# Kernel tuning notes

Measured on AMD Instinct MI355X. Metric: run time of the kernel, lower is better.

## Reference

```python
import jax, jax.numpy as jnp
import numpy as np

N_NODES = 50000
N_EDGES = 600000
IN_CH = 128
HID = 256
OUT_FEAT = 256
OUT_CH = 128
EPS = 1e-12


def _sage_conv(x, src, dst, mask_f, Wl, bl, Wr, n_nodes):
    # PyG SAGEConv: out = lin_l(mean_{j in N(i)} x_j) + lin_r(x_i); L2-normalize rows.
    msg = x[src] * mask_f[:, None]                                  # [E, d] gather
    agg = jax.ops.segment_sum(msg, dst, num_segments=n_nodes)      # [N, d]
    cnt = jax.ops.segment_sum(mask_f, dst, num_segments=n_nodes)   # [N]
    agg = agg / jnp.maximum(cnt, 1.0)[:, None]                      # mean over kept edges
    out = agg @ Wl.T + bl + x @ Wr.T                                 # [N, h]
    nrm = jnp.maximum(jnp.linalg.norm(out, axis=-1, keepdims=True), EPS)
    return out / nrm


def setup_inputs() -> dict:
    key = jax.random.key(0)
    ks = jax.random.split(key, 12)
    x = jax.random.normal(ks[0], (N_NODES, IN_CH), dtype=jnp.float32)
    edge_index = jax.random.randint(ks[1], (2, N_EDGES), 0, N_NODES, dtype=jnp.int32)
    edge_mask = jax.random.bernoulli(ks[2], 0.7, (N_EDGES,))  # dropout_edge p=0.3 keep mask

    def lin(k, fan_out, fan_in):
        s = 1.0 / np.sqrt(fan_in)
        return jax.random.uniform(k, (fan_out, fan_in), jnp.float32, -s, s)

    W1l = lin(ks[3], HID, IN_CH)
    b1 = jnp.zeros((HID,), jnp.float32)
    W1r = lin(ks[4], HID, IN_CH)
    Ws = lin(ks[5], HID, IN_CH)
    bs = jnp.zeros((HID,), jnp.float32)
    W2l = lin(ks[6], OUT_FEAT, HID)
    b2 = jnp.zeros((OUT_FEAT,), jnp.float32)
    W2r = lin(ks[7], OUT_FEAT, HID)
    Wo = lin(ks[8], OUT_CH, OUT_FEAT)
    bo = jnp.zeros((OUT_CH,), jnp.float32)
    return {"x": x, "edge_index": edge_index, "edge_mask": edge_mask,
            "W1l": W1l, "b1": b1, "W1r": W1r, "Ws": Ws, "bs": bs,
            "W2l": W2l, "b2": b2, "W2r": W2r, "Wo": Wo, "bo": bo}


def reference(x, edge_index, edge_mask, W1l, b1, W1r, Ws, bs, W2l, b2, W2r, Wo, bo):
    src, dst = edge_index[0], edge_index[1]
    ones = jnp.ones((src.shape[0],), x.dtype)
    # conv1 uses all edges
    h = _sage_conv(x, src, dst, ones, W1l, b1, W1r, N_NODES)
    h = h + (x @ Ws.T + bs)
    h = jnp.tanh(h)
    # conv2 uses edge-dropped graph (mask = kept edges)
    mask_f = edge_mask.astype(x.dtype)
    h = jnp.tanh(_sage_conv(h, src, dst, mask_f, W2l, b2, W2r, N_NODES))
    return h @ Wo.T + bo
```

## Files before the change

kernel.cpp:

```cpp
#include <hip/hip_runtime.h>
#include <hip/hip_bf16.h>

#define N_NODES 50000
#define N_PAD   50048
#define N_EDGES 600000
#define IN_CH 128
#define HID 256
#define OUT_CH 128

typedef unsigned short u16;
typedef unsigned char u8;
typedef unsigned int u32;

typedef __attribute__((ext_vector_type(8))) short short8;
typedef __attribute__((ext_vector_type(4))) float f32x4;

typedef __attribute__((address_space(3))) u32 as3_u32;
typedef __attribute__((address_space(1))) const u32 as1_u32;

__device__ __forceinline__ float bf2f(u16 v) {
    unsigned u = ((unsigned)v) << 16;
    return __uint_as_float(u);
}
__device__ __forceinline__ u16 f2bf(float f) {
    unsigned u = __float_as_uint(f);
    u += 0x7FFF + ((u >> 16) & 1);
    return (u16)(u >> 16);
}

__device__ __forceinline__ void async16(const void* g, void* l) {
    __builtin_amdgcn_global_load_lds((as1_u32*)g, (as3_u32*)l, 16, 0, 0);
}

__global__ void detect_kernel(const u16* __restrict__ xu, const u8* __restrict__ mb,
                              int* __restrict__ flags) {
    int lane = threadIdx.x & 63;

    int inr = 0;
    {
        u32 w0 = ((const u32*)xu)[lane * 2 + 0];
        u32 w1 = ((const u32*)xu)[lane * 2 + 1];
        u16 h[4] = {(u16)w0, (u16)(w0 >> 16), (u16)w1, (u16)(w1 >> 16)};
#pragma unroll
        for (int j = 0; j < 4; j++) {
            int e = (h[j] >> 7) & 0xFF;
            if (e >= 100 && e <= 133) inr++;
        }
    }

    int c1 = 0, c23 = 0, h3f_1 = 0, h3f_3 = 0;
#pragma unroll
    for (int t = 0; t < 16; t++) {
        u32 w = ((const u32*)mb)[t * 64 + lane];
        u8 b1 = (u8)(w >> 8), b2 = (u8)(w >> 16), b3 = (u8)(w >> 24);
        if (b1) c1++;
        if (b1 == 0x3F) h3f_1 = 1;
        if (b2) c23++;
        if (b3) c23++;
        if (b3 == 0x3F) h3f_3 = 1;
    }

#pragma unroll
    for (int off = 32; off > 0; off >>= 1) {
        inr   += __shfl_xor(inr, off, 64);
        c1    += __shfl_xor(c1, off, 64);
        c23   += __shfl_xor(c23, off, 64);
        h3f_1 |= __shfl_xor(h3f_1, off, 64);
        h3f_3 |= __shfl_xor(h3f_3, off, 64);
    }

    if (lane == 0 && blockIdx.x == 0) {
        flags[0] = (inr >= 200) ? 1 : 0;
        int fmt;
        if (h3f_1) fmt = 3;
        else if (h3f_3) fmt = 2;
        else if (c1 + c23 > 0) fmt = 0;
        else fmt = 1;
        flags[1] = fmt;
    }
}

__global__ void biases_kernel(const void* __restrict__ b1, const void* __restrict__ bs,
                              const void* __restrict__ b2, const void* __restrict__ bo,
                              float* __restrict__ dst, const int* __restrict__ flags) {
    int i = blockIdx.x * blockDim.x + threadIdx.x;
    if (i >= 896) return;
    const void* src; int idx;
    if (i < 256)      { src = b1; idx = i; }
    else if (i < 512) { src = bs; idx = i - 256; }
    else if (i < 768) { src = b2; idx = i - 512; }
    else              { src = bo; idx = i - 768; }
    float v;
    if (flags[0]) v = bf2f(((const u16*)src)[idx]);
    else          v = ((const float*)src)[idx];
    dst[i] = v;
}

__global__ void wcat_kernel(const void* __restrict__ A, const void* __restrict__ B,
                            u16* __restrict__ dst, int N, int K1, int K2,
                            const int* __restrict__ flags) {
    int i = blockIdx.x * blockDim.x + threadIdx.x;
    int K = K1 + K2;
    if (i >= N * K) return;
    int n = i / K, k = i % K;
    const void* src; int idx;
    if (k < K1) { src = A; idx = n * K1 + k; }
    else        { src = B; idx = n * K2 + (k - K1); }
    u16 v;
    if (flags[0]) v = ((const u16*)src)[idx];
    else          v = f2bf(((const float*)src)[idx]);
    dst[i] = v;
}

__global__ void hist_kernel(const int* __restrict__ ei, int* __restrict__ deg,
                            int* __restrict__ rank) {
    int i = blockIdx.x * blockDim.x + threadIdx.x;
    if (i >= N_EDGES) return;
    int d = ei[N_EDGES + i];
    rank[i] = atomicAdd(&deg[d], 1);
}

__global__ void partial_kernel(const int* __restrict__ deg, int* __restrict__ partial) {
    __shared__ int sh[256];
    int t = threadIdx.x;
    int i = blockIdx.x * 256 + t;
    sh[t] = (i < N_NODES) ? deg[i] : 0;
    __syncthreads();
    for (int s = 128; s > 0; s >>= 1) {
        if (t < s) sh[t] += sh[t + s];
        __syncthreads();
    }
    if (t == 0) partial[blockIdx.x] = sh[0];
}

__global__ void scanp_kernel(const int* __restrict__ partial, int* __restrict__ pscan, int nb) {
    __shared__ int sh[256];
    int t = threadIdx.x;
    int v = (t < nb) ? partial[t] : 0;
    sh[t] = v;
    __syncthreads();
    for (int o = 1; o < 256; o <<= 1) {
        int u = (t >= o) ? sh[t - o] : 0;
        __syncthreads();
        sh[t] += u;
        __syncthreads();
    }
    if (t < nb) pscan[t] = sh[t] - v;
}

__global__ void rowptr_kernel(const int* __restrict__ deg, const int* __restrict__ pscan,
                              int* __restrict__ row_ptr) {
    __shared__ int sh[256];
    int t = threadIdx.x;
    int i = blockIdx.x * 256 + t;
    int v = (i < N_NODES) ? deg[i] : 0;
    sh[t] = v;
    __syncthreads();
    for (int o = 1; o < 256; o <<= 1) {
        int u = (t >= o) ? sh[t - o] : 0;
        __syncthreads();
        sh[t] += u;
        __syncthreads();
    }
    if (i <= N_NODES) row_ptr[i] = pscan[blockIdx.x] + sh[t] - v;
}

__global__ void scatter_csr_kernel(const int* __restrict__ ei, const int* __restrict__ rank,
                                   const int* __restrict__ row_ptr,
                                   const void* __restrict__ em,
                                   u32* __restrict__ srcs, const int* __restrict__ flags) {
    int i = blockIdx.x * blockDim.x + threadIdx.x;
    if (i >= N_EDGES) return;
    int d = ei[N_EDGES + i];
    int p = row_ptr[d] + rank[i];
    int fmt = flags[1];
    bool keep;
    if (fmt == 0)      keep = ((const u8*)em)[i] != 0;
    else if (fmt == 1) keep = ((const int*)em)[i] != 0;
    else if (fmt == 2) keep = ((const float*)em)[i] != 0.f;
    else               keep = ((const u16*)em)[i] != 0;
    srcs[p] = (u32)ei[i] | (keep ? 0u : 0x80000000u);
}

__global__ __launch_bounds__(256) void gather1_kernel(const int* __restrict__ row_ptr,
                                                      const u32* __restrict__ srcs,
                                                      const u16* __restrict__ xb,
                                                      u16* __restrict__ aggb) {
    int wid = (blockIdx.x * blockDim.x + threadIdx.x) >> 6;
    int lane = threadIdx.x & 63;
    if (wid >= N_NODES) return;
    int start = row_ptr[wid], end = row_ptr[wid + 1];
    float ax = 0.f, ay = 0.f, bx = 0.f, by = 0.f;
    int e = start;
    for (; e + 2 <= end; e += 2) {
        int s0 = (int)(srcs[e] & 0x7fffffffu);
        int s1 = (int)(srcs[e + 1] & 0x7fffffffu);
        u32 v0 = *(const u32*)(xb + (size_t)s0 * IN_CH + lane * 2);
        u32 v1 = *(const u32*)(xb + (size_t)s1 * IN_CH + lane * 2);
        ax += bf2f((u16)v0); ay += bf2f((u16)(v0 >> 16));
        bx += bf2f((u16)v1); by += bf2f((u16)(v1 >> 16));
    }
    if (e < end) {
        int s0 = (int)(srcs[e] & 0x7fffffffu);
        u32 v0 = *(const u32*)(xb + (size_t)s0 * IN_CH + lane * 2);
        ax += bf2f((u16)v0); ay += bf2f((u16)(v0 >> 16));
    }
    float inv = 1.f / fmaxf((float)(end - start), 1.f);
    u32 o = (u32)f2bf((ax + bx) * inv) | ((u32)f2bf((ay + by) * inv) << 16);
    *(u32*)(aggb + (size_t)wid * IN_CH + lane * 2) = o;
}

__global__ __launch_bounds__(256) void gather2_kernel(const int* __restrict__ row_ptr,
                                                      const u32* __restrict__ srcs,
                                                      const u16* __restrict__ h1b,
                                                      u16* __restrict__ aggb) {
    int wid = (blockIdx.x * blockDim.x + threadIdx.x) >> 6;
    int lane = threadIdx.x & 63;
    if (wid >= N_NODES) return;
    int start = row_ptr[wid], end = row_ptr[wid + 1];
    float a0 = 0.f, a1 = 0.f, a2 = 0.f, a3 = 0.f, c = 0.f;
    for (int e = start; e < end; e++) {
        u32 sv = srcs[e];
        if ((int)sv >= 0) {
            const u16* p = h1b + (size_t)sv * HID + lane * 4;
            u32 v0 = *(const u32*)p;
            u32 v1 = *(const u32*)(p + 2);
            a0 += bf2f((u16)v0);
            a1 += bf2f((u16)(v0 >> 16));
            a2 += bf2f((u16)v1);
            a3 += bf2f((u16)(v1 >> 16));
            c += 1.f;
        }
    }
    float inv = 1.f / fmaxf(c, 1.f);
    u32 o0 = (u32)f2bf(a0 * inv) | ((u32)f2bf(a1 * inv) << 16);
    u32 o1 = (u32)f2bf(a2 * inv) | ((u32)f2bf(a3 * inv) << 16);
    u16* p = aggb + (size_t)wid * HID + lane * 4;
    *(u32*)p = o0;
    *(u32*)(p + 2) = o1;
}

template<int MODE>
__global__ __launch_bounds__(256, 2) void gemm_staged(
    const u16* __restrict__ A0, const u16* __restrict__ A1,
    const u16* __restrict__ W0, const u16* __restrict__ W1,
    const float* __restrict__ bias0, const float* __restrict__ bias1,
    u16* __restrict__ outb, void* __restrict__ outv, const int* __restrict__ flags) {

    constexpr int NT  = (MODE == 3) ? 2 : 4;
    constexpr int Nw  = NT * 16;
    constexpr int NKS = (MODE == 1) ? 6 : ((MODE == 2) ? 8 : 4);
    constexpr int BBYTES = NT * 64 * 128;
    __shared__ __align__(16) u8 ldsmem[16384 + 2 * BBYTES];

    int tid = threadIdx.x;
    int w = tid >> 6, lane = tid & 63;
    int q = lane >> 4, c = lane & 15;
    int m_base = blockIdx.x * 64;
    int rj = lane >> 3, jj = lane & 7;
    int j16 = ((jj ^ rj) << 4);

    f32x4 acc[4][NT], acc2[4][NT];
    const f32x4 z = {0.f, 0.f, 0.f, 0.f};
#pragma unroll
    for (int mt = 0; mt < 4; mt++)
#pragma unroll
        for (int nt = 0; nt < NT; nt++) { acc[mt][nt] = z; acc2[mt][nt] = z; }

    auto stage = [&](int ks, int b) {
        const u16* ap; int astr, kta;
        const u16* wp; int wstr, ktw;
        if (MODE == 1) {
            astr = 128;
            if (ks < 2)      { ap = A0; kta = ks; }
            else if (ks < 4) { ap = A1; kta = ks - 2; }
            else             { ap = A1; kta = ks - 4; }
            if (ks < 4) { wp = W0; wstr = 256; ktw = ks; }
            else        { wp = W1; wstr = 128; ktw = ks - 4; }
        } else if (MODE == 2) {
            astr = 256;
            if (ks < 4) { ap = A0; kta = ks; } else { ap = A1; kta = ks - 4; }
            wp = W0; wstr = 512; ktw = ks;
        } else {
            astr = 256; ap = A0; kta = ks;
            wp = W0; wstr = 256; ktw = ks;
        }
#pragma unroll
        for (int t = 0; t < 2; t++) {
            int r = w * 16 + t * 8;
            const u8* g = (const u8*)(ap + (size_t)(m_base + r + rj) * astr) + kta * 128 + j16;
            async16(g, ldsmem + b * 8192 + r * 128);
        }
#pragma unroll
        for (int t = 0; t < NT * 2; t++) {
            int n = w * Nw + t * 8;
            const u8* g = (const u8*)(wp + (size_t)(n + rj) * wstr) + ktw * 128 + j16;
            async16(g, ldsmem + 16384 + b * BBYTES + n * 128);
        }
    };

    auto compute = [&](int b, f32x4 (*tgt)[NT]) {
        const u8* ab = ldsmem + b * 8192;
        const u8* bb = ldsmem + 16384 + b * BBYTES;
#pragma unroll
        for (int kk = 0; kk < 2; kk++) {
            int sA = (((kk * 4 + q) ^ (c & 7)) << 4);
            short8 af[4], bfr[NT];
#pragma unroll
            for (int mt = 0; mt < 4; mt++)
                af[mt] = *(const short8*)(ab + (mt * 16 + c) * 128 + sA);
#pragma unroll
            for (int nt = 0; nt < NT; nt++)
                bfr[nt] = *(const short8*)(bb + (w * Nw + nt * 16 + c) * 128 + sA);
#pragma unroll
            for (int mt = 0; mt < 4; mt++)
#pragma unroll
                for (int nt = 0; nt < NT; nt++)
                    tgt[mt][nt] = __builtin_amdgcn_mfma_f32_16x16x32_bf16(af[mt], bfr[nt], tgt[mt][nt], 0, 0, 0);
        }
    };

    stage(0, 0);
    int b = 0;
#pragma unroll
    for (int ks = 0; ks < NKS; ks++) {
        __syncthreads();
        if (ks + 1 < NKS) stage(ks + 1, b ^ 1);
        if (MODE == 1 && ks >= 4) compute(b, acc2);
        else                      compute(b, acc);
        b ^= 1;
    }
    __syncthreads();

    if (MODE == 3) {
        float bcol[NT];
#pragma unroll
        for (int nt = 0; nt < NT; nt++) bcol[nt] = bias0[w * Nw + nt * 16 + c];
        int isbf = flags[0];
#pragma unroll
        for (int mt = 0; mt < 4; mt++)
#pragma unroll
            for (int r = 0; r < 4; r++) {
                int row = m_base + mt * 16 + q * 4 + r;
                if (row < N_NODES) {
#pragma unroll
                    for (int nt = 0; nt < NT; nt++) {
                        float v = acc[mt][nt][r] + bcol[nt];
                        int col = w * Nw + nt * 16 + c;
                        if (isbf) ((u16*)outv)[(size_t)row * OUT_CH + col] = f2bf(v);
                        else      ((float*)outv)[(size_t)row * OUT_CH + col] = v;
                    }
                }
            }
    } else {
        float* redf = (float*)ldsmem;
        float bcol[NT], b2col[NT];
#pragma unroll
        for (int nt = 0; nt < NT; nt++) {
            int col = w * Nw + nt * 16 + c;
            bcol[nt] = bias0[col];
            if (MODE == 1) b2col[nt] = bias1[col];
        }
        float s[4][4];
#pragma unroll
        for (int mt = 0; mt < 4; mt++)
#pragma unroll
            for (int r = 0; r < 4; r++) {
                float t = 0.f;
#pragma unroll
                for (int nt = 0; nt < NT; nt++) {
                    float v = acc[mt][nt][r] + bcol[nt];
                    acc[mt][nt][r] = v;
                    t += v * v;
                }
                s[mt][r] = t;
            }
#pragma unroll
        for (int off = 1; off < 16; off <<= 1) {
#pragma unroll
            for (int mt = 0; mt < 4; mt++)
#pragma unroll
                for (int r = 0; r < 4; r++)
                    s[mt][r] += __shfl_xor(s[mt][r], off, 64);
        }
        if (c == 0) {
#pragma unroll
            for (int mt = 0; mt < 4; mt++)
#pragma unroll
                for (int r = 0; r < 4; r++)
                    redf[(mt * 16 + q * 4 + r) * 4 + w] = s[mt][r];
        }
        __syncthreads();
        if (tid < 64) {
            float t = redf[tid * 4] + redf[tid * 4 + 1] + redf[tid * 4 + 2] + redf[tid * 4 + 3];
            redf[256 + tid] = 1.f / fmaxf(sqrtf(t), 1e-12f);
        }
        __syncthreads();
#pragma unroll
        for (int mt = 0; mt < 4; mt++)
#pragma unroll
            for (int r = 0; r < 4; r++) {
                int rl = mt * 16 + q * 4 + r;
                int row = m_base + rl;
                if (row < N_NODES) {
                    float iv = redf[256 + rl];
#pragma unroll
                    for (int nt = 0; nt < NT; nt++) {
                        int col = w * Nw + nt * 16 + c;
                        float h;
                        if (MODE == 1) h = acc[mt][nt][r] * iv + acc2[mt][nt][r] + b2col[nt];
                        else           h = acc[mt][nt][r] * iv;
                        outb[(size_t)row * HID + col] = f2bf(tanhf(h));
                    }
                }
            }
    }
}

extern "C" void kernel_launch(void* const* d_in, const int* in_sizes, int n_in,
                              void* d_out, int out_size, void* d_ws, size_t ws_size,
                              hipStream_t stream) {
    const void* x    = d_in[0];
    const int*  ei   = (const int*)d_in[1];
    const void* em   = d_in[2];
    const void* W1l  = d_in[3];
    const void* b1   = d_in[4];
    const void* W1r  = d_in[5];
    const void* Ws   = d_in[6];
    const void* bs   = d_in[7];
    const void* W2l  = d_in[8];
    const void* b2   = d_in[9];
    const void* W2r  = d_in[10];
    const void* Wo   = d_in[11];
    const void* bo   = d_in[12];

    char* p = (char*)d_ws;
    auto carve = [&](size_t bytes) { char* r = p; p += (bytes + 63) & ~(size_t)63; return r; };
    int*   flags  = (int*)carve(256);
    u16*   xb     = (u16*)carve((size_t)N_PAD * IN_CH * 2);
    u16*   h1b    = (u16*)carve((size_t)N_PAD * HID * 2);
    u16*   aggb   = (u16*)carve((size_t)N_PAD * HID * 2);
    u16*   h2b    = (u16*)carve((size_t)N_PAD * HID * 2);
    u16*   Wc1    = (u16*)carve(256 * 256 * 2);
    u16*   Wsb    = (u16*)carve(256 * 128 * 2);
    u16*   Wc2    = (u16*)carve(256 * 512 * 2);
    u16*   Wob    = (u16*)carve(128 * 256 * 2);
    float* biasf  = (float*)carve(896 * 4);
    int*   deg    = (int*)carve(50056 * 4);
    int*   row_ptr= (int*)carve(50056 * 4);
    int*   partial= (int*)carve(256 * 4);
    int*   pscan  = (int*)carve(256 * 4);
    int*   rank   = (int*)carve((size_t)N_EDGES * 4);
    u32*   srcs   = (u32*)carve((size_t)N_EDGES * 4);
    float* b1f = biasf, *bsf = biasf + 256, *b2f = biasf + 512, *bof = biasf + 768;
    (void)ws_size; (void)in_sizes; (void)n_in; (void)out_size;

    detect_kernel<<<1, 64, 0, stream>>>((const u16*)x, (const u8*)em, flags);

    wcat_kernel<<<(N_NODES * IN_CH + 255) / 256, 256, 0, stream>>>(x, x, xb, 1, N_NODES * IN_CH, 0, flags);
    wcat_kernel<<<(256 * 256 + 255) / 256, 256, 0, stream>>>(W1l, W1r, Wc1, 256, 128, 128, flags);
    wcat_kernel<<<(256 * 128 + 255) / 256, 256, 0, stream>>>(Ws, Ws, Wsb, 1, 256 * 128, 0, flags);
    wcat_kernel<<<(256 * 512 + 255) / 256, 256, 0, stream>>>(W2l, W2r, Wc2, 256, 256, 256, flags);
    wcat_kernel<<<(128 * 256 + 255) / 256, 256, 0, stream>>>(Wo, Wo, Wob, 1, 128 * 256, 0, flags);
    biases_kernel<<<4, 256, 0, stream>>>(b1, bs, b2, bo, biasf, flags);

    hipMemsetAsync(deg, 0, 50056 * sizeof(int), stream);
    hist_kernel<<<(N_EDGES + 255) / 256, 256, 0, stream>>>(ei, deg, rank);
    const int NB = (N_NODES + 255) / 256;
    partial_kernel<<<NB, 256, 0, stream>>>(deg, partial);
    scanp_kernel<<<1, 256, 0, stream>>>(partial, pscan, NB);
    rowptr_kernel<<<NB, 256, 0, stream>>>(deg, pscan, row_ptr);
    scatter_csr_kernel<<<(N_EDGES + 255) / 256, 256, 0, stream>>>(ei, rank, row_ptr, em, srcs, flags);

    const int GB = N_PAD / 64;

    gather1_kernel<<<(N_NODES * 64) / 256, 256, 0, stream>>>(row_ptr, srcs, xb, aggb);
    gemm_staged<1><<<GB, 256, 0, stream>>>(aggb, xb, Wc1, Wsb, b1f, bsf, h1b, nullptr, flags);

    gather2_kernel<<<(N_NODES * 64) / 256, 256, 0, stream>>>(row_ptr, srcs, h1b, aggb);
    gemm_staged<2><<<GB, 256, 0, stream>>>(aggb, h1b, Wc2, nullptr, b2f, nullptr, h2b, nullptr, flags);

    gemm_staged<3><<<GB, 256, 0, stream>>>(h2b, nullptr, Wob, nullptr, bof, nullptr, nullptr, d_out, flags);
}
```

Measured before the change: 352.0 us.

## Build separate masked CSR and preload neighbor indices per wave with readlane

Builds a second CSR containing only kept edges, so the second gather no longer branches on a mask bit per edge and drops masked edges entirely. Both gather kernels load up to 64 neighbor indices in one coalesced per-lane read and broadcast them with readlane instead of issuing scalar loads per edge. The second gather also unrolls by two with uint2 loads to get more memory requests in flight. In exchange the CSR build does a second atomic histogram, doubles the scan work and writes an extra index array.

```diff
diff --git a/kernel.cpp b/kernel.cpp
--- a/kernel.cpp
+++ b/kernel.cpp
@@ -112,129 +112,166 @@
     dst[i] = v;
 }
 
-__global__ void hist_kernel(const int* __restrict__ ei, int* __restrict__ deg,
-                            int* __restrict__ rank) {
+__global__ void hist_kernel(const int* __restrict__ ei, const void* __restrict__ em,
+                            int* __restrict__ deg, int* __restrict__ deg2,
+                            int* __restrict__ rank, int* __restrict__ krank,
+                            const int* __restrict__ flags) {
     int i = blockIdx.x * blockDim.x + threadIdx.x;
     if (i >= N_EDGES) return;
     int d = ei[N_EDGES + i];
     rank[i] = atomicAdd(&deg[d], 1);
-}
-
-__global__ void partial_kernel(const int* __restrict__ deg, int* __restrict__ partial) {
-    __shared__ int sh[256];
-    int t = threadIdx.x;
-    int i = blockIdx.x * 256 + t;
-    sh[t] = (i < N_NODES) ? deg[i] : 0;
-    __syncthreads();
-    for (int s = 128; s > 0; s >>= 1) {
-        if (t < s) sh[t] += sh[t + s];
-        __syncthreads();
-    }
-    if (t == 0) partial[blockIdx.x] = sh[0];
-}
-
-__global__ void scanp_kernel(const int* __restrict__ partial, int* __restrict__ pscan, int nb) {
-    __shared__ int sh[256];
-    int t = threadIdx.x;
-    int v = (t < nb) ? partial[t] : 0;
-    sh[t] = v;
-    __syncthreads();
-    for (int o = 1; o < 256; o <<= 1) {
-        int u = (t >= o) ? sh[t - o] : 0;
-        __syncthreads();
-        sh[t] += u;
-        __syncthreads();
-    }
-    if (t < nb) pscan[t] = sh[t] - v;
-}
-
-__global__ void rowptr_kernel(const int* __restrict__ deg, const int* __restrict__ pscan,
-                              int* __restrict__ row_ptr) {
-    __shared__ int sh[256];
-    int t = threadIdx.x;
-    int i = blockIdx.x * 256 + t;
-    int v = (i < N_NODES) ? deg[i] : 0;
-    sh[t] = v;
-    __syncthreads();
-    for (int o = 1; o < 256; o <<= 1) {
-        int u = (t >= o) ? sh[t - o] : 0;
-        __syncthreads();
-        sh[t] += u;
-        __syncthreads();
-    }
-    if (i <= N_NODES) row_ptr[i] = pscan[blockIdx.x] + sh[t] - v;
-}
-
-__global__ void scatter_csr_kernel(const int* __restrict__ ei, const int* __restrict__ rank,
-                                   const int* __restrict__ row_ptr,
-                                   const void* __restrict__ em,
-                                   u32* __restrict__ srcs, const int* __restrict__ flags) {
-    int i = blockIdx.x * blockDim.x + threadIdx.x;
-    if (i >= N_EDGES) return;
-    int d = ei[N_EDGES + i];
-    int p = row_ptr[d] + rank[i];
     int fmt = flags[1];
     bool keep;
     if (fmt == 0)      keep = ((const u8*)em)[i] != 0;
     else if (fmt == 1) keep = ((const int*)em)[i] != 0;
     else if (fmt == 2) keep = ((const float*)em)[i] != 0.f;
     else               keep = ((const u16*)em)[i] != 0;
-    srcs[p] = (u32)ei[i] | (keep ? 0u : 0x80000000u);
+    krank[i] = keep ? atomicAdd(&deg2[d], 1) : -1;
+}
+
+__global__ void partial_kernel(const int* __restrict__ deg, const int* __restrict__ deg2,
+                               int* __restrict__ partial, int nb) {
+    __shared__ int sh[256];
+    int t = threadIdx.x;
+    int arr = (blockIdx.x >= nb) ? 1 : 0;
+    int blk = blockIdx.x - arr * nb;
+    const int* d = arr ? deg2 : deg;
+    int i = blk * 256 + t;
+    sh[t] = (i < N_NODES) ? d[i] : 0;
+    __syncthreads();
+    for (int s = 128; s > 0; s >>= 1) {
+        if (t < s) sh[t] += sh[t + s];
+        __syncthreads();
+    }
+    if (t == 0) partial[blockIdx.x] = sh[0];
+}
+
+__global__ void scanp_kernel(const int* __restrict__ partial, int* __restrict__ pscan, int nb) {
+    __shared__ int sh[256];
+    int t = threadIdx.x;
+    int base = blockIdx.x * nb;
+    int v = (t < nb) ? partial[base + t] : 0;
+    sh[t] = v;
+    __syncthreads();
+    for (int o = 1; o < 256; o <<= 1) {
+        int u = (t >= o) ? sh[t - o] : 0;
+        __syncthreads();
+        sh[t] += u;
+        __syncthreads();
+    }
+    if (t < nb) pscan[base + t] = sh[t] - v;
+}
+
+__global__ void rowptr_kernel(const int* __restrict__ deg, const int* __restrict__ deg2,
+                              const int* __restrict__ pscan,
+                              int* __restrict__ row_ptr, int* __restrict__ row_ptr2, int nb) {
+    __shared__ int sh[256];
+    int t = threadIdx.x;
+    int arr = (blockIdx.x >= nb) ? 1 : 0;
+    int blk = blockIdx.x - arr * nb;
+    const int* d = arr ? deg2 : deg;
+    int* rp = arr ? row_ptr2 : row_ptr;
+    int i = blk * 256 + t;
+    int v = (i < N_NODES) ? d[i] : 0;
+    sh[t] = v;
+    __syncthreads();
+    for (int o = 1; o < 256; o <<= 1) {
+        int u = (t >= o) ? sh[t - o] : 0;
+        __syncthreads();
+        sh[t] += u;
+        __syncthreads();
+    }
+    if (i <= N_NODES) rp[i] = pscan[arr * nb + blk] + sh[t] - v;
+}
+
+__global__ void scatter_csr_kernel(const int* __restrict__ ei, const int* __restrict__ rank,
+                                   const int* __restrict__ krank,
+                                   const int* __restrict__ row_ptr, const int* __restrict__ row_ptr2,
+                                   int* __restrict__ srcs, int* __restrict__ srcs2) {
+    int i = blockIdx.x * blockDim.x + threadIdx.x;
+    if (i >= N_EDGES) return;
+    int d = ei[N_EDGES + i];
+    int s = ei[i];
+    srcs[row_ptr[d] + rank[i]] = s;
+    int r2 = krank[i];
+    if (r2 >= 0) srcs2[row_ptr2[d] + r2] = s;
 }
 
 __global__ __launch_bounds__(256) void gather1_kernel(const int* __restrict__ row_ptr,
-                                                      const u32* __restrict__ srcs,
+                                                      const int* __restrict__ srcs,
                                                       const u16* __restrict__ xb,
                                                       u16* __restrict__ aggb) {
     int wid = (blockIdx.x * blockDim.x + threadIdx.x) >> 6;
     int lane = threadIdx.x & 63;
     if (wid >= N_NODES) return;
     int start = row_ptr[wid], end = row_ptr[wid + 1];
+    int dg = end - start;
+    int sv = (lane < dg) ? srcs[start + lane] : 0;
     float ax = 0.f, ay = 0.f, bx = 0.f, by = 0.f;
-    int e = start;
-    for (; e + 2 <= end; e += 2) {
-        int s0 = (int)(srcs[e] & 0x7fffffffu);
-        int s1 = (int)(srcs[e + 1] & 0x7fffffffu);
+    int n = dg < 64 ? dg : 64;
+    int e = 0;
+    for (; e + 2 <= n; e += 2) {
+        int s0 = __builtin_amdgcn_readlane(sv, e);
+        int s1 = __builtin_amdgcn_readlane(sv, e + 1);
         u32 v0 = *(const u32*)(xb + (size_t)s0 * IN_CH + lane * 2);
         u32 v1 = *(const u32*)(xb + (size_t)s1 * IN_CH + lane * 2);
         ax += bf2f((u16)v0); ay += bf2f((u16)(v0 >> 16));
         bx += bf2f((u16)v1); by += bf2f((u16)(v1 >> 16));
     }
-    if (e < end) {
-        int s0 = (int)(srcs[e] & 0x7fffffffu);
+    if (e < n) {
+        int s0 = __builtin_amdgcn_readlane(sv, e);
         u32 v0 = *(const u32*)(xb + (size_t)s0 * IN_CH + lane * 2);
         ax += bf2f((u16)v0); ay += bf2f((u16)(v0 >> 16));
     }
-    float inv = 1.f / fmaxf((float)(end - start), 1.f);
+    for (e = 64; e < dg; e++) {
+        int s0 = srcs[start + e];
+        u32 v0 = *(const u32*)(xb + (size_t)s0 * IN_CH + lane * 2);
+        ax += bf2f((u16)v0); ay += bf2f((u16)(v0 >> 16));
+    }
+    float inv = 1.f / fmaxf((float)dg, 1.f);
     u32 o = (u32)f2bf((ax + bx) * inv) | ((u32)f2bf((ay + by) * inv) << 16);
     *(u32*)(aggb + (size_t)wid * IN_CH + lane * 2) = o;
 }
 
-__global__ __launch_bounds__(256) void gather2_kernel(const int* __restrict__ row_ptr,
-                                                      const u32* __restrict__ srcs,
+__global__ __launch_bounds__(256) void gather2_kernel(const int* __restrict__ row_ptr2,
+                                                      const int* __restrict__ srcs2,
                                                       const u16* __restrict__ h1b,
                                                       u16* __restrict__ aggb) {
     int wid = (blockIdx.x * blockDim.x + threadIdx.x) >> 6;
     int lane = threadIdx.x & 63;
     if (wid >= N_NODES) return;
-    int start = row_ptr[wid], end = row_ptr[wid + 1];
-    float a0 = 0.f, a1 = 0.f, a2 = 0.f, a3 = 0.f, c = 0.f;
-    for (int e = start; e < end; e++) {
-        u32 sv = srcs[e];
-        if ((int)sv >= 0) {
-            const u16* p = h1b + (size_t)sv * HID + lane * 4;
-            u32 v0 = *(const u32*)p;
-            u32 v1 = *(const u32*)(p + 2);
-            a0 += bf2f((u16)v0);
-            a1 += bf2f((u16)(v0 >> 16));
-            a2 += bf2f((u16)v1);
-            a3 += bf2f((u16)(v1 >> 16));
-            c += 1.f;
-        }
-    }
-    float inv = 1.f / fmaxf(c, 1.f);
-    u32 o0 = (u32)f2bf(a0 * inv) | ((u32)f2bf(a1 * inv) << 16);
-    u32 o1 = (u32)f2bf(a2 * inv) | ((u32)f2bf(a3 * inv) << 16);
+    int start = row_ptr2[wid], end = row_ptr2[wid + 1];
+    int dg = end - start;
+    int sv = (lane < dg) ? srcs2[start + lane] : 0;
+    float a0 = 0.f, a1 = 0.f, a2 = 0.f, a3 = 0.f;
+    float b0 = 0.f, b1 = 0.f, b2 = 0.f, b3 = 0.f;
+    int n = dg < 64 ? dg : 64;
+    int e = 0;
+    for (; e + 2 <= n; e += 2) {
+        int s0 = __builtin_amdgcn_readlane(sv, e);
+        int s1 = __builtin_amdgcn_readlane(sv, e + 1);
+        uint2 v = *(const uint2*)(h1b + (size_t)s0 * HID + lane * 4);
+        uint2 w = *(const uint2*)(h1b + (size_t)s1 * HID + lane * 4);
+        a0 += bf2f((u16)v.x); a1 += bf2f((u16)(v.x >> 16));
+        a2 += bf2f((u16)v.y); a3 += bf2f((u16)(v.y >> 16));
+        b0 += bf2f((u16)w.x); b1 += bf2f((u16)(w.x >> 16));
+        b2 += bf2f((u16)w.y); b3 += bf2f((u16)(w.y >> 16));
+    }
+    if (e < n) {
+        int s0 = __builtin_amdgcn_readlane(sv, e);
+        uint2 v = *(const uint2*)(h1b + (size_t)s0 * HID + lane * 4);
+        a0 += bf2f((u16)v.x); a1 += bf2f((u16)(v.x >> 16));
+        a2 += bf2f((u16)v.y); a3 += bf2f((u16)(v.y >> 16));
+    }
+    for (e = 64; e < dg; e++) {
+        int s0 = srcs2[start + e];
+        uint2 v = *(const uint2*)(h1b + (size_t)s0 * HID + lane * 4);
+        a0 += bf2f((u16)v.x); a1 += bf2f((u16)(v.x >> 16));
+        a2 += bf2f((u16)v.y); a3 += bf2f((u16)(v.y >> 16));
+    }
+    float inv = 1.f / fmaxf((float)dg, 1.f);
+    u32 o0 = (u32)f2bf((a0 + b0) * inv) | ((u32)f2bf((a1 + b1) * inv) << 16);
+    u32 o1 = (u32)f2bf((a2 + b2) * inv) | ((u32)f2bf((a3 + b3) * inv) << 16);
     u16* p = aggb + (size_t)wid * HID + lane * 4;
     *(u32*)p = o0;
     *(u32*)(p + 2) = o1;
@@ -436,22 +473,26 @@
 
     char* p = (char*)d_ws;
     auto carve = [&](size_t bytes) { char* r = p; p += (bytes + 63) & ~(size_t)63; return r; };
-    int*   flags  = (int*)carve(256);
-    u16*   xb     = (u16*)carve((size_t)N_PAD * IN_CH * 2);
-    u16*   h1b    = (u16*)carve((size_t)N_PAD * HID * 2);
-    u16*   aggb   = (u16*)carve((size_t)N_PAD * HID * 2);
-    u16*   h2b    = (u16*)carve((size_t)N_PAD * HID * 2);
-    u16*   Wc1    = (u16*)carve(256 * 256 * 2);
-    u16*   Wsb    = (u16*)carve(256 * 128 * 2);
-    u16*   Wc2    = (u16*)carve(256 * 512 * 2);
-    u16*   Wob    = (u16*)carve(128 * 256 * 2);
-    float* biasf  = (float*)carve(896 * 4);
-    int*   deg    = (int*)carve(50056 * 4);
-    int*   row_ptr= (int*)carve(50056 * 4);
-    int*   partial= (int*)carve(256 * 4);
-    int*   pscan  = (int*)carve(256 * 4);
-    int*   rank   = (int*)carve((size_t)N_EDGES * 4);
-    u32*   srcs   = (u32*)carve((size_t)N_EDGES * 4);
+    int*   flags   = (int*)carve(256);
+    u16*   xb      = (u16*)carve((size_t)N_PAD * IN_CH * 2);
+    u16*   h1b     = (u16*)carve((size_t)N_PAD * HID * 2);
+    u16*   aggb    = (u16*)carve((size_t)N_PAD * HID * 2);
+    u16*   h2b     = (u16*)carve((size_t)N_PAD * HID * 2);
+    u16*   Wc1     = (u16*)carve(256 * 256 * 2);
+    u16*   Wsb     = (u16*)carve(256 * 128 * 2);
+    u16*   Wc2     = (u16*)carve(256 * 512 * 2);
+    u16*   Wob     = (u16*)carve(128 * 256 * 2);
+    float* biasf   = (float*)carve(896 * 4);
+    int*   deg     = (int*)carve(2 * 50176 * 4);
+    int*   deg2    = deg + 50176;
+    int*   row_ptr = (int*)carve(50056 * 4);
+    int*   row_ptr2= (int*)carve(50056 * 4);
+    int*   partial = (int*)carve(512 * 4);
+    int*   pscan   = (int*)carve(512 * 4);
+    int*   rank    = (int*)carve((size_t)N_EDGES * 4);
+    int*   krank   = (int*)carve((size_t)N_EDGES * 4);
+    int*   srcs    = (int*)carve((size_t)N_EDGES * 4);
+    int*   srcs2   = (int*)carve((size_t)N_EDGES * 4);
     float* b1f = biasf, *bsf = biasf + 256, *b2f = biasf + 512, *bof = biasf + 768;
     (void)ws_size; (void)in_sizes; (void)n_in; (void)out_size;
 
@@ -464,20 +505,20 @@
     wcat_kernel<<<(128 * 256 + 255) / 256, 256, 0, stream>>>(Wo, Wo, Wob, 1, 128 * 256, 0, flags);
     biases_kernel<<<4, 256, 0, stream>>>(b1, bs, b2, bo, biasf, flags);
 
-    hipMemsetAsync(deg, 0, 50056 * sizeof(int), stream);
-    hist_kernel<<<(N_EDGES + 255) / 256, 256, 0, stream>>>(ei, deg, rank);
+    hipMemsetAsync(deg, 0, 2 * 50176 * sizeof(int), stream);
+    hist_kernel<<<(N_EDGES + 255) / 256, 256, 0, stream>>>(ei, em, deg, deg2, rank, krank, flags);
     const int NB = (N_NODES + 255) / 256;
-    partial_kernel<<<NB, 256, 0, stream>>>(deg, partial);
-    scanp_kernel<<<1, 256, 0, stream>>>(partial, pscan, NB);
-    rowptr_kernel<<<NB, 256, 0, stream>>>(deg, pscan, row_ptr);
-    scatter_csr_kernel<<<(N_EDGES + 255) / 256, 256, 0, stream>>>(ei, rank, row_ptr, em, srcs, flags);
+    partial_kernel<<<2 * NB, 256, 0, stream>>>(deg, deg2, partial, NB);
+    scanp_kernel<<<2, 256, 0, stream>>>(partial, pscan, NB);
+    rowptr_kernel<<<2 * NB, 256, 0, stream>>>(deg, deg2, pscan, row_ptr, row_ptr2, NB);
+    scatter_csr_kernel<<<(N_EDGES + 255) / 256, 256, 0, stream>>>(ei, rank, krank, row_ptr, row_ptr2, srcs, srcs2);
 
     const int GB = N_PAD / 64;
 
     gather1_kernel<<<(N_NODES * 64) / 256, 256, 0, stream>>>(row_ptr, srcs, xb, aggb);
     gemm_staged<1><<<GB, 256, 0, stream>>>(aggb, xb, Wc1, Wsb, b1f, bsf, h1b, nullptr, flags);
 
-    gather2_kernel<<<(N_NODES * 64) / 256, 256, 0, stream>>>(row_ptr, srcs, h1b, aggb);
+    gather2_kernel<<<(N_NODES * 64) / 256, 256, 0, stream>>>(row_ptr2, srcs2, h1b, aggb);
     gemm_staged<2><<<GB, 256, 0, stream>>>(aggb, h1b, Wc2, nullptr, b2f, nullptr, h2b, nullptr, flags);
 
     gemm_staged<3><<<GB, 256, 0, stream>>>(h2b, nullptr, Wob, nullptr, bof, nullptr, nullptr, d_out, flags);
```

After: 339.2 us. -3.6%, faster.
